# Optimization experiments

Measured on AMD Instinct MI355X. Metric: run time of the kernel, lower is better.

Reference implementation:

```python
import jax, jax.numpy as jnp
import numpy as np

B, S, D, H, DFF = 4, 2048, 512, 8, 2048
DK = D // H
EPS = 1e-6
NEG = -1.0e9


def _linear(x, w, b):
    return x @ w.T + b


def _layernorm(x, gamma, bias):
    # torch.var default is unbiased (ddof=1); gamma/bias are scalars
    mean = jnp.mean(x, axis=-1, keepdims=True)
    var = jnp.var(x, axis=-1, keepdims=True, ddof=1)
    return gamma * (x - mean) / jnp.sqrt(var + EPS) + bias


def setup_inputs() -> dict:
    key = jax.random.key(0)
    ks = jax.random.split(key, 16)
    sc = 0.02
    inp = {
        "x": jax.random.normal(ks[0], (B, S, D), jnp.float32),
        "mask": jax.random.randint(ks[1], (B, 1, 1, S), 0, 2).astype(jnp.bool_),
        "wq": jax.random.normal(ks[2], (D, D), jnp.float32) * sc,
        "bq": jnp.zeros((D,), jnp.float32),
        "wk": jax.random.normal(ks[3], (D, D), jnp.float32) * sc,
        "bk": jnp.zeros((D,), jnp.float32),
        "wv": jax.random.normal(ks[4], (D, D), jnp.float32) * sc,
        "bv": jnp.zeros((D,), jnp.float32),
        "wo": jax.random.normal(ks[5], (D, D), jnp.float32) * sc,
        "bo": jnp.zeros((D,), jnp.float32),
        "w1": jax.random.normal(ks[6], (DFF, D), jnp.float32) * sc,
        "b1": jnp.zeros((DFF,), jnp.float32),
        "w2": jax.random.normal(ks[7], (D, DFF), jnp.float32) * sc,
        "b2": jnp.zeros((D,), jnp.float32),
        "g1": jnp.ones((), jnp.float32),
        "beta1": jnp.zeros((), jnp.float32),
        "g2": jnp.ones((), jnp.float32),
        "beta2": jnp.zeros((), jnp.float32),
    }
    return inp


def reference(x, mask, wq, bq, wk, bk, wv, bv, wo, bo, w1, b1, w2, b2, g1, beta1, g2, beta2):
    # --- multi-head self-attention ---
    q = _linear(x, wq, bq).reshape(B, S, H, DK)
    k = _linear(x, wk, bk).reshape(B, S, H, DK)
    v = _linear(x, wv, bv).reshape(B, S, H, DK)
    scores = jnp.einsum("bqhd,bkhd->bhqk", q, k) / jnp.sqrt(jnp.float32(DK))
    scores = jnp.where(mask, NEG, scores)  # masked_fill_ where mask is True
    attn = jax.nn.softmax(scores, axis=-1)
    o = jnp.einsum("bhqk,bkhd->bqhd", attn, v).reshape(B, S, D)
    attn_out = _linear(o, wo, bo)
    # skip connection 1: x + norm(sublayer_out)  (dropout = identity at inference)
    y = x + _layernorm(attn_out, g1, beta1)
    # --- feed-forward ---
    ff = _linear(jax.nn.relu(_linear(y, w1, b1)), w2, b2)
    # skip connection 2
    return y + _layernorm(ff, g2, beta2)
```

## Files before the change

kernel.cpp:

```cpp
#include <hip/hip_runtime.h>
#include <hip/hip_bf16.h>
#include <math.h>

#define B_ 4
#define S_ 2048
#define D_ 512
#define H_ 8
#define DK_ 64
#define DFF_ 2048
#define NEG_ (-1.0e9f)
#define EPS_ 1e-6f

typedef __attribute__((ext_vector_type(8))) short bf16x8;
typedef __attribute__((ext_vector_type(4))) float f32x4;

__device__ inline unsigned short f2bf(float f) {
    unsigned u = __float_as_uint(f);
    unsigned r = u + 0x7FFFu + ((u >> 16) & 1u);
    return (unsigned short)(r >> 16);
}

__device__ inline f32x4 mfma16(bf16x8 a, bf16x8 b, f32x4 c) {
    return __builtin_amdgcn_mfma_f32_16x16x32_bf16(a, b, c, 0, 0, 0);
}

__device__ inline void gload16(const void* g, void* l) {
    __builtin_amdgcn_global_load_lds(
        (const __attribute__((address_space(1))) unsigned int*)g,
        (__attribute__((address_space(3))) unsigned int*)l, 16, 0, 0);
}
__device__ inline void gload4(const void* g, void* l) {
    __builtin_amdgcn_global_load_lds(
        (const __attribute__((address_space(1))) unsigned int*)g,
        (__attribute__((address_space(3))) unsigned int*)l, 4, 0, 0);
}

__global__ void mask_canon_kernel(const unsigned char* __restrict__ mraw,
                                  float* __restrict__ mb) {
    __shared__ int s_bad;
    int tid = threadIdx.x;
    if (tid == 0) s_bad = 0;
    __syncthreads();
    const unsigned int* w = (const unsigned int*)mraw;
    int bad = 0;
    for (int i = tid; i < (B_ * S_) / 4; i += 256) {
        unsigned int v = w[i];
        if (!(v == 0u || v == 1u || v == 0x3F800000u)) bad = 1;
    }
    if (bad) atomicOr(&s_bad, 1);
    __syncthreads();
    int i = blockIdx.x * 256 + tid;
    if (s_bad) {
        for (; i < B_ * S_; i += 2048) mb[i] = mraw[i] ? NEG_ : 0.f;
    } else {
        for (; i < B_ * S_; i += 2048) mb[i] = w[i] ? NEG_ : 0.f;
    }
}

__global__ __launch_bounds__(256) void convert_all_kernel(
    const float* __restrict__ x,  const float* __restrict__ wq,
    const float* __restrict__ wk, const float* __restrict__ wv,
    const float* __restrict__ wo, const float* __restrict__ w1,
    const float* __restrict__ w2,
    unsigned short* __restrict__ xb, unsigned short* __restrict__ wqkvb,
    unsigned short* __restrict__ wob, unsigned short* __restrict__ w1b,
    unsigned short* __restrict__ w2b)
{
    int i = blockIdx.x * 256 + threadIdx.x;
    const float* src; unsigned short* dst; int off; float s = 1.f;
    if (i < 1048576)      { src = x;  dst = xb;             off = i;           }
    else if (i < 1114112) { src = wq; dst = wqkvb;          off = i - 1048576; s = 0.125f; }
    else if (i < 1179648) { src = wk; dst = wqkvb + 262144; off = i - 1114112; }
    else if (i < 1245184) { src = wv; dst = wqkvb + 524288; off = i - 1179648; }
    else if (i < 1310720) { src = wo; dst = wob;            off = i - 1245184; }
    else if (i < 1572864) { src = w1; dst = w1b;            off = i - 1310720; }
    else                  { src = w2; dst = w2b;            off = i - 1572864; }
    float4 v = reinterpret_cast<const float4*>(src)[off];
    ushort4 o;
    o.x = f2bf(v.x * s); o.y = f2bf(v.y * s); o.z = f2bf(v.z * s); o.w = f2bf(v.w * s);
    reinterpret_cast<ushort4*>(dst)[off] = o;
}

template<int BM, int BN, bool RELU, bool OUT_BF16>
__global__ __launch_bounds__(256) void gemm_mfma(
    const unsigned short* __restrict__ A, const unsigned short* __restrict__ W,
    const float* __restrict__ bias, void* __restrict__ Cout,
    int M, int N, int K)
{
    constexpr int FM = BM / 32;
    constexpr int FN = BN / 32;
    __shared__ unsigned short Asl[BM * 64];
    __shared__ unsigned short Bsl[BN * 64];

    const int tid = threadIdx.x;
    const int w = tid >> 6, lane = tid & 63;
    const int lr = lane & 15, lg = lane >> 4;
    const int wm = w >> 1, wn = w & 1;
    const int m0 = blockIdx.y * BM, n0 = blockIdx.x * BN;
    const int srow = lane >> 3;
    const int schunk = lane & 7;

    f32x4 acc[FM][FN] = {};

    for (int k0 = 0; k0 < K; k0 += 64) {
        __syncthreads();
        #pragma unroll
        for (int j = 0; j < BM / 32; ++j) {
            int instr = w * (BM / 32) + j;
            int row = instr * 8 + srow;
            const unsigned short* src =
                A + (size_t)(m0 + row) * K + k0 + ((schunk ^ (row & 7)) * 8);
            gload16(src, &Asl[instr * 512]);
        }
        #pragma unroll
        for (int j = 0; j < BN / 32; ++j) {
            int instr = w * (BN / 32) + j;
            int row = instr * 8 + srow;
            const unsigned short* src =
                W + (size_t)(n0 + row) * K + k0 + ((schunk ^ (row & 7)) * 8);
            gload16(src, &Bsl[instr * 512]);
        }
        __syncthreads();

        bf16x8 af[FM][2], bfr[FN][2];
        #pragma unroll
        for (int m = 0; m < FM; ++m)
            #pragma unroll
            for (int ko = 0; ko < 2; ++ko) {
                int row = wm * (FM * 16) + m * 16 + lr;
                int slot = (lg + 4 * ko) ^ (row & 7);
                af[m][ko] = *(const bf16x8*)&Asl[row * 64 + slot * 8];
            }
        #pragma unroll
        for (int n = 0; n < FN; ++n)
            #pragma unroll
            for (int ko = 0; ko < 2; ++ko) {
                int row = wn * (FN * 16) + n * 16 + lr;
                int slot = (lg + 4 * ko) ^ (row & 7);
                bfr[n][ko] = *(const bf16x8*)&Bsl[row * 64 + slot * 8];
            }
        #pragma unroll
        for (int m = 0; m < FM; ++m)
            #pragma unroll
            for (int n = 0; n < FN; ++n)
                #pragma unroll
                for (int ko = 0; ko < 2; ++ko)
                    acc[m][n] = mfma16(af[m][ko], bfr[n][ko], acc[m][n]);
    }

    #pragma unroll
    for (int n = 0; n < FN; ++n) {
        int col = n0 + wn * (FN * 16) + n * 16 + lr;
        float bv = bias[col];
        #pragma unroll
        for (int m = 0; m < FM; ++m) {
            int rowb = m0 + wm * (FM * 16) + m * 16 + lg * 4;
            #pragma unroll
            for (int r = 0; r < 4; ++r) {
                float v = acc[m][n][r] + bv;
                if (RELU) v = fmaxf(v, 0.f);
                if (OUT_BF16)
                    ((unsigned short*)Cout)[(size_t)(rowb + r) * N + col] = f2bf(v);
                else
                    ((float*)Cout)[(size_t)(rowb + r) * N + col] = v;
            }
        }
    }
}

__global__ __launch_bounds__(256) void gemm_qkv(
    const unsigned short* __restrict__ A, const unsigned short* __restrict__ W,
    const float* __restrict__ bqp, const float* __restrict__ bkp,
    const float* __restrict__ bvp, unsigned short* __restrict__ QKb,
    unsigned short* __restrict__ VTg)
{
    constexpr int K = 512;
    __shared__ unsigned short Asl[128 * 64];
    __shared__ unsigned short Bsl[128 * 64];

    const int tid = threadIdx.x;
    const int w = tid >> 6, lane = tid & 63;
    const int lr = lane & 15, lg = lane >> 4;
    const int wm = w >> 1, wn = w & 1;
    const int m0 = blockIdx.y * 128, n0 = blockIdx.x * 128;
    const int srow = lane >> 3;
    const int schunk = lane & 7;

    f32x4 acc[4][4] = {};

    for (int k0 = 0; k0 < K; k0 += 64) {
        __syncthreads();
        #pragma unroll
        for (int j = 0; j < 4; ++j) {
            int instr = w * 4 + j;
            int row = instr * 8 + srow;
            gload16(A + (size_t)(m0 + row) * K + k0 + ((schunk ^ (row & 7)) * 8),
                    &Asl[instr * 512]);
            gload16(W + (size_t)(n0 + row) * K + k0 + ((schunk ^ (row & 7)) * 8),
                    &Bsl[instr * 512]);
        }
        __syncthreads();

        bf16x8 af[4][2], bfr[4][2];
        #pragma unroll
        for (int m = 0; m < 4; ++m)
            #pragma unroll
            for (int ko = 0; ko < 2; ++ko) {
                int row = wm * 64 + m * 16 + lr;
                int slot = (lg + 4 * ko) ^ (row & 7);
                af[m][ko] = *(const bf16x8*)&Asl[row * 64 + slot * 8];
            }
        #pragma unroll
        for (int n = 0; n < 4; ++n)
            #pragma unroll
            for (int ko = 0; ko < 2; ++ko) {
                int row = wn * 64 + n * 16 + lr;
                int slot = (lg + 4 * ko) ^ (row & 7);
                bfr[n][ko] = *(const bf16x8*)&Bsl[row * 64 + slot * 8];
            }
        #pragma unroll
        for (int m = 0; m < 4; ++m)
            #pragma unroll
            for (int n = 0; n < 4; ++n)
                #pragma unroll
                for (int ko = 0; ko < 2; ++ko)
                    acc[m][n] = mfma16(af[m][ko], bfr[n][ko], acc[m][n]);
    }

    if (n0 < 1024) {
        #pragma unroll
        for (int n = 0; n < 4; ++n) {
            int col = n0 + wn * 64 + n * 16 + lr;
            float bv = (col < 512) ? bqp[col] * 0.125f : bkp[col - 512];
            #pragma unroll
            for (int m = 0; m < 4; ++m) {
                int rowb = m0 + wm * 64 + m * 16 + lg * 4;
                #pragma unroll
                for (int r = 0; r < 4; ++r)
                    QKb[(size_t)(rowb + r) * 1024 + col] = f2bf(acc[m][n][r] + bv);
            }
        }
    } else {
        #pragma unroll
        for (int n = 0; n < 4; ++n) {
            int col = n0 + wn * 64 + n * 16 + lr;
            int dfull = col - 1024;
            int hh = dfull >> 6, dd = dfull & 63;
            float bv = bvp[dfull];
            #pragma unroll
            for (int m = 0; m < 4; ++m) {
                int rowb = m0 + wm * 64 + m * 16 + lg * 4;
                int bb = rowb >> 11;
                int s = rowb & 2047;
                ushort4 pk;
                pk.x = f2bf(acc[m][n][0] + bv);
                pk.y = f2bf(acc[m][n][1] + bv);
                pk.z = f2bf(acc[m][n][2] + bv);
                pk.w = f2bf(acc[m][n][3] + bv);
                *(ushort4*)&VTg[(((size_t)bb * 8 + hh) * 64 + dd) * 2048 + s] = pk;
            }
        }
    }
}

__global__ __launch_bounds__(256, 4) void attn_mfma3(
    const unsigned short* __restrict__ QKb, const unsigned short* __restrict__ VTg,
    const float* __restrict__ mb, unsigned short* __restrict__ Ob)
{
    __shared__ unsigned short Ks[64 * 64];
    __shared__ unsigned short VTs[64 * 64];
    __shared__ unsigned short Ps[4 * 16 * 64];
    __shared__ float Ms[64];

    const int tid = threadIdx.x;
    const int w = tid >> 6, lane = tid & 63;
    const int lr = lane & 15, lg = lane >> 4;
    const int flat = blockIdx.x + 32 * (blockIdx.y + 8 * blockIdx.z);
    const int nf = (flat & 7) * 128 + (flat >> 3);
    const int q0 = (nf & 31) * 64;
    const int bh = nf >> 5;
    const int h = bh & 7, b = bh >> 3;
    const int srow = lane >> 3;
    const int sc_x = (lane & 7) ^ srow;
    unsigned short* PsW = &Ps[w * 1024];

    bf16x8 qf[2];
    #pragma unroll
    for (int ko = 0; ko < 2; ++ko)
        qf[ko] = *(const bf16x8*)(QKb +
            (size_t)(b * S_ + q0 + w * 16 + lr) * 1024 + h * 64 + ko * 32 + lg * 8);

    f32x4 od[4] = {};
    float m_run = -INFINITY;
    float l_run = 0.f;

    for (int kv0 = 0; kv0 < S_; kv0 += 64) {
        __syncthreads();
        #pragma unroll
        for (int j = 0; j < 2; ++j) {
            int rl = w * 16 + j * 8 + srow;
            gload16(QKb + (size_t)(b * S_ + kv0 + rl) * 1024 + 512 + h * 64 + sc_x * 8,
                    &Ks[(w * 2 + j) * 512]);
            gload16(VTg + ((size_t)bh * 64 + rl) * 2048 + kv0 + sc_x * 8,
                    &VTs[(w * 2 + j) * 512]);
        }
        if (w == 0) gload4(mb + (size_t)b * S_ + kv0 + lane, Ms);
        __syncthreads();

        f32x4 st[4] = {};
        #pragma unroll
        for (int ko = 0; ko < 2; ++ko)
            #pragma unroll
            for (int n = 0; n < 4; ++n) {
                bf16x8 kf = *(const bf16x8*)
                    &Ks[(n * 16 + lr) * 64 + (((lg + 4 * ko) ^ (lr & 7)) * 8)];
                st[n] = mfma16(kf, qf[ko], st[n]);
            }

        float mtp = -INFINITY;
        #pragma unroll
        for (int n = 0; n < 4; ++n) {
            f32x4 mbr = *(const f32x4*)&Ms[n * 16 + lg * 4];
            #pragma unroll
            for (int r = 0; r < 4; ++r) {
                float v = st[n][r] + mbr[r];
                st[n][r] = v;
                mtp = fmaxf(mtp, v);
            }
        }

        if (__any(mtp > m_run + 4.f)) {
            float mt = mtp;
            mt = fmaxf(mt, __shfl_xor(mt, 16));
            mt = fmaxf(mt, __shfl_xor(mt, 32));
            float mnew = fmaxf(m_run, mt);
            float scl = __expf(m_run - mnew);
            m_run = mnew;
            l_run *= scl;
            #pragma unroll
            for (int r = 0; r < 4; ++r) {
                float sr = __shfl(scl, lg * 4 + r);
                #pragma unroll
                for (int nd = 0; nd < 4; ++nd) od[nd][r] *= sr;
            }
        }

        float psum = 0.f;
        #pragma unroll
        for (int n = 0; n < 4; ++n) {
            float p0 = __expf(st[n][0] - m_run);
            float p1 = __expf(st[n][1] - m_run);
            float p2 = __expf(st[n][2] - m_run);
            float p3 = __expf(st[n][3] - m_run);
            psum += (p0 + p1) + (p2 + p3);
            ushort4 pk;
            pk.x = f2bf(p0); pk.y = f2bf(p1); pk.z = f2bf(p2); pk.w = f2bf(p3);
            int chunk = (2 * n + (lg >> 1)) ^ (lr & 7);
            *(ushort4*)&PsW[lr * 64 + chunk * 8 + (lg & 1) * 4] = pk;
        }
        psum += __shfl_xor(psum, 16);
        psum += __shfl_xor(psum, 32);
        l_run += psum;

        #pragma unroll
        for (int ko = 0; ko < 2; ++ko) {
            int slotx = ((lg + 4 * ko) ^ (lr & 7)) * 8;
            bf16x8 pa = *(const bf16x8*)&PsW[lr * 64 + slotx];
            #pragma unroll
            for (int nd = 0; nd < 4; ++nd) {
                bf16x8 vf = *(const bf16x8*)&VTs[(nd * 16 + lr) * 64 + slotx];
                od[nd] = mfma16(pa, vf, od[nd]);
            }
        }
    }

    float linv = 1.f / l_run;
    #pragma unroll
    for (int r = 0; r < 4; ++r) {
        float iv = __shfl(linv, lg * 4 + r);
        size_t row = (size_t)(b * S_ + q0 + w * 16 + lg * 4 + r);
        #pragma unroll
        for (int nd = 0; nd < 4; ++nd)
            Ob[row * 512 + h * 64 + nd * 16 + lr] = f2bf(od[nd][r] * iv);
    }
}

__global__ __launch_bounds__(256) void add_ln_kernel(
    const float* __restrict__ x, const float* __restrict__ a,
    const float* __restrict__ g, const float* __restrict__ beta,
    float* __restrict__ y, unsigned short* __restrict__ ybf)
{
    int rowid = blockIdx.x;
    int tid = threadIdx.x;
    const float2 a2 = reinterpret_cast<const float2*>(a + (size_t)rowid * D_)[tid];
    float s = a2.x + a2.y;
    float ss = a2.x * a2.x + a2.y * a2.y;
    #pragma unroll
    for (int off = 32; off > 0; off >>= 1) {
        s += __shfl_down(s, off);
        ss += __shfl_down(ss, off);
    }
    __shared__ float ws_s[4], ws_ss[4];
    __shared__ float s_mean, s_rstd;
    int wave = tid >> 6, lane = tid & 63;
    if (lane == 0) { ws_s[wave] = s; ws_ss[wave] = ss; }
    __syncthreads();
    if (tid == 0) {
        float st = ws_s[0] + ws_s[1] + ws_s[2] + ws_s[3];
        float sst = ws_ss[0] + ws_ss[1] + ws_ss[2] + ws_ss[3];
        float mean = st / (float)D_;
        float var = (sst - (float)D_ * mean * mean) / (float)(D_ - 1);
        s_mean = mean;
        s_rstd = rsqrtf(var + EPS_);
    }
    __syncthreads();
    float mean = s_mean, rstd = s_rstd, gg = g[0], bb = beta[0];
    const float2 x2 = reinterpret_cast<const float2*>(x + (size_t)rowid * D_)[tid];
    float2 o;
    o.x = x2.x + gg * (a2.x - mean) * rstd + bb;
    o.y = x2.y + gg * (a2.y - mean) * rstd + bb;
    reinterpret_cast<float2*>(y + (size_t)rowid * D_)[tid] = o;
    if (ybf) {
        ushort2 ob; ob.x = f2bf(o.x); ob.y = f2bf(o.y);
        reinterpret_cast<ushort2*>(ybf + (size_t)rowid * D_)[tid] = ob;
    }
}

extern "C" void kernel_launch(void* const* d_in, const int* in_sizes, int n_in,
                              void* d_out, int out_size, void* d_ws, size_t ws_size,
                              hipStream_t stream) {
    const float* x  = (const float*)d_in[0];
    const unsigned char* mask = (const unsigned char*)d_in[1];
    const float* wq = (const float*)d_in[2];
    const float* bq = (const float*)d_in[3];
    const float* wk = (const float*)d_in[4];
    const float* bk = (const float*)d_in[5];
    const float* wv = (const float*)d_in[6];
    const float* bv = (const float*)d_in[7];
    const float* wo = (const float*)d_in[8];
    const float* bo = (const float*)d_in[9];
    const float* w1 = (const float*)d_in[10];
    const float* b1 = (const float*)d_in[11];
    const float* w2 = (const float*)d_in[12];
    const float* b2 = (const float*)d_in[13];
    const float* g1 = (const float*)d_in[14];
    const float* be1 = (const float*)d_in[15];
    const float* g2 = (const float*)d_in[16];
    const float* be2 = (const float*)d_in[17];
    float* out = (float*)d_out;
    char* base = (char*)d_ws;

    const size_t MS = (size_t)B_ * S_;
    unsigned short* QKb  = (unsigned short*)(base);
    unsigned short* VTg  = (unsigned short*)(base + 16777216);
    unsigned short* Ob   = (unsigned short*)(base + 25165824);
    unsigned short* ff1  = (unsigned short*)(base);
    float*          att  = (float*)(base + 33554432);
    float*          ff2  = att;
    float*          y    = (float*)(base + 50331648);
    unsigned short* ybf  = (unsigned short*)(base + 67108864);
    unsigned short* xb   = (unsigned short*)(base + 75497472);
    unsigned short* wqkvb= (unsigned short*)(base + 83886080);
    unsigned short* wob  = (unsigned short*)(base + 85458944);
    unsigned short* w1b  = (unsigned short*)(base + 85983232);
    unsigned short* w2b  = (unsigned short*)(base + 88080384);
    float*          mbv  = (float*)(base + 90183680);

    dim3 blk(256);
    mask_canon_kernel<<<8, blk, 0, stream>>>(mask, mbv);

    convert_all_kernel<<<7168, blk, 0, stream>>>(
        x, wq, wk, wv, wo, w1, w2, xb, wqkvb, wob, w1b, w2b);

    gemm_qkv<<<dim3(12, MS / 128), blk, 0, stream>>>(
        xb, wqkvb, bq, bk, bv, QKb, VTg);

    attn_mfma3<<<dim3(S_ / 64, H_, B_), blk, 0, stream>>>(QKb, VTg, mbv, Ob);

    gemm_mfma<128,64,false,false><<<dim3(D_/64, MS/128), blk, 0, stream>>>(
        Ob, wob, bo, att, MS, D_, D_);

    add_ln_kernel<<<dim3((unsigned)MS), blk, 0, stream>>>(x, att, g1, be1, y, ybf);

    gemm_mfma<128,128,true,true><<<dim3(DFF_/128, MS/128), blk, 0, stream>>>(
        ybf, w1b, b1, ff1, MS, DFF_, D_);
    gemm_mfma<128,64,false,false><<<dim3(D_/64, MS/128), blk, 0, stream>>>(
        ff1, w2b, b2, ff2, MS, D_, DFF_);

    add_ln_kernel<<<dim3((unsigned)MS), blk, 0, stream>>>(y, ff2, g2, be2, out, nullptr);
}
```

Before: 296.8 us.

## Double-buffer attention K/V tiles, use exp2 softmax, and remap GEMM blocks across XCDs

The attention kernel now double-buffers K and V^T tiles in LDS and prefetches the next tile while computing the current one, so one barrier per iteration replaces two. The mask bias is read straight from global memory instead of staged through LDS. The softmax runs in base 2: log2(e) is folded into the Q weight and bias scaling, exp2f replaces __expf, and the rescale threshold is raised. Probabilities are packed to bf16 with paired conversions, and the GEMM block indices are permuted so neighbouring tiles spread across the 8 XCDs for better L2 locality. The cost is doubled LDS for K/V, which may limit occupancy.

```diff
diff --git a/kernel.cpp b/kernel.cpp
--- a/kernel.cpp
+++ b/kernel.cpp
@@ -10,6 +10,7 @@
 #define DFF_ 2048
 #define NEG_ (-1.0e9f)
 #define EPS_ 1e-6f
+#define LOG2E_ 1.4426950408889634f
 
 typedef __attribute__((ext_vector_type(8))) short bf16x8;
 typedef __attribute__((ext_vector_type(4))) float f32x4;
@@ -20,6 +21,13 @@
     return (unsigned short)(r >> 16);
 }
 
+__device__ inline unsigned int packbf2(float a, float b) {
+    __hip_bfloat162 h = __float22bfloat162_rn(float2{a, b});
+    unsigned int u;
+    __builtin_memcpy(&u, &h, 4);
+    return u;
+}
+
 __device__ inline f32x4 mfma16(bf16x8 a, bf16x8 b, f32x4 c) {
     return __builtin_amdgcn_mfma_f32_16x16x32_bf16(a, b, c, 0, 0, 0);
 }
@@ -28,11 +36,6 @@
     __builtin_amdgcn_global_load_lds(
         (const __attribute__((address_space(1))) unsigned int*)g,
         (__attribute__((address_space(3))) unsigned int*)l, 16, 0, 0);
-}
-__device__ inline void gload4(const void* g, void* l) {
-    __builtin_amdgcn_global_load_lds(
-        (const __attribute__((address_space(1))) unsigned int*)g,
-        (__attribute__((address_space(3))) unsigned int*)l, 4, 0, 0);
 }
 
 __global__ void mask_canon_kernel(const unsigned char* __restrict__ mraw,
@@ -69,7 +72,7 @@
     int i = blockIdx.x * 256 + threadIdx.x;
     const float* src; unsigned short* dst; int off; float s = 1.f;
     if (i < 1048576)      { src = x;  dst = xb;             off = i;           }
-    else if (i < 1114112) { src = wq; dst = wqkvb;          off = i - 1048576; s = 0.125f; }
+    else if (i < 1114112) { src = wq; dst = wqkvb;          off = i - 1048576; s = 0.125f * LOG2E_; }
     else if (i < 1179648) { src = wk; dst = wqkvb + 262144; off = i - 1114112; }
     else if (i < 1245184) { src = wv; dst = wqkvb + 524288; off = i - 1179648; }
     else if (i < 1310720) { src = wo; dst = wob;            off = i - 1245184; }
@@ -96,7 +99,11 @@
     const int w = tid >> 6, lane = tid & 63;
     const int lr = lane & 15, lg = lane >> 4;
     const int wm = w >> 1, wn = w & 1;
-    const int m0 = blockIdx.y * BM, n0 = blockIdx.x * BN;
+    const int gx = gridDim.x;
+    const int flat = blockIdx.y * gx + blockIdx.x;
+    const int cpx = (gx * gridDim.y) >> 3;
+    const int nf = (flat & 7) * cpx + (flat >> 3);
+    const int m0 = (nf / gx) * BM, n0 = (nf % gx) * BN;
     const int srow = lane >> 3;
     const int schunk = lane & 7;
 
@@ -182,7 +189,9 @@
     const int w = tid >> 6, lane = tid & 63;
     const int lr = lane & 15, lg = lane >> 4;
     const int wm = w >> 1, wn = w & 1;
-    const int m0 = blockIdx.y * 128, n0 = blockIdx.x * 128;
+    const int flat = blockIdx.y * 12 + blockIdx.x;
+    const int nf = (flat & 7) * 96 + (flat >> 3);
+    const int m0 = (nf / 12) * 128, n0 = (nf % 12) * 128;
     const int srow = lane >> 3;
     const int schunk = lane & 7;
 
@@ -231,7 +240,7 @@
         #pragma unroll
         for (int n = 0; n < 4; ++n) {
             int col = n0 + wn * 64 + n * 16 + lr;
-            float bv = (col < 512) ? bqp[col] * 0.125f : bkp[col - 512];
+            float bv = (col < 512) ? bqp[col] * (0.125f * LOG2E_) : bkp[col - 512];
             #pragma unroll
             for (int m = 0; m < 4; ++m) {
                 int rowb = m0 + wm * 64 + m * 16 + lg * 4;
@@ -263,14 +272,28 @@
     }
 }
 
-__global__ __launch_bounds__(256, 4) void attn_mfma3(
+__device__ inline void stage_kv(const unsigned short* __restrict__ QKb,
+                                const unsigned short* __restrict__ VTg,
+                                unsigned short* ksDst, unsigned short* vtDst,
+                                int b, int bh, int h, int kv0,
+                                int w, int srow, int sc_x) {
+    #pragma unroll
+    for (int j = 0; j < 2; ++j) {
+        int rl = w * 16 + j * 8 + srow;
+        gload16(QKb + (size_t)(b * S_ + kv0 + rl) * 1024 + 512 + h * 64 + sc_x * 8,
+                ksDst + (w * 2 + j) * 512);
+        gload16(VTg + ((size_t)bh * 64 + rl) * 2048 + kv0 + sc_x * 8,
+                vtDst + (w * 2 + j) * 512);
+    }
+}
+
+__global__ __launch_bounds__(256, 4) void attn_mfma4(
     const unsigned short* __restrict__ QKb, const unsigned short* __restrict__ VTg,
     const float* __restrict__ mb, unsigned short* __restrict__ Ob)
 {
-    __shared__ unsigned short Ks[64 * 64];
-    __shared__ unsigned short VTs[64 * 64];
+    __shared__ unsigned short Ks[2][64 * 64];
+    __shared__ unsigned short VTs[2][64 * 64];
     __shared__ unsigned short Ps[4 * 16 * 64];
-    __shared__ float Ms[64];
 
     const int tid = threadIdx.x;
     const int w = tid >> 6, lane = tid & 63;
@@ -294,18 +317,19 @@
     float m_run = -INFINITY;
     float l_run = 0.f;
 
+    stage_kv(QKb, VTg, Ks[0], VTs[0], b, bh, h, 0, w, srow, sc_x);
+    __syncthreads();
+
+    int cur = 0;
     for (int kv0 = 0; kv0 < S_; kv0 += 64) {
-        __syncthreads();
-        #pragma unroll
-        for (int j = 0; j < 2; ++j) {
-            int rl = w * 16 + j * 8 + srow;
-            gload16(QKb + (size_t)(b * S_ + kv0 + rl) * 1024 + 512 + h * 64 + sc_x * 8,
-                    &Ks[(w * 2 + j) * 512]);
-            gload16(VTg + ((size_t)bh * 64 + rl) * 2048 + kv0 + sc_x * 8,
-                    &VTs[(w * 2 + j) * 512]);
-        }
-        if (w == 0) gload4(mb + (size_t)b * S_ + kv0 + lane, Ms);
-        __syncthreads();
+        if (kv0 + 64 < S_)
+            stage_kv(QKb, VTg, Ks[cur ^ 1], VTs[cur ^ 1], b, bh, h, kv0 + 64,
+                     w, srow, sc_x);
+
+        f32x4 mbr[4];
+        #pragma unroll
+        for (int n = 0; n < 4; ++n)
+            mbr[n] = *(const f32x4*)&mb[(size_t)b * S_ + kv0 + n * 16 + lg * 4];
 
         f32x4 st[4] = {};
         #pragma unroll
@@ -313,28 +337,26 @@
             #pragma unroll
             for (int n = 0; n < 4; ++n) {
                 bf16x8 kf = *(const bf16x8*)
-                    &Ks[(n * 16 + lr) * 64 + (((lg + 4 * ko) ^ (lr & 7)) * 8)];
+                    &Ks[cur][(n * 16 + lr) * 64 + (((lg + 4 * ko) ^ (lr & 7)) * 8)];
                 st[n] = mfma16(kf, qf[ko], st[n]);
             }
 
         float mtp = -INFINITY;
         #pragma unroll
-        for (int n = 0; n < 4; ++n) {
-            f32x4 mbr = *(const f32x4*)&Ms[n * 16 + lg * 4];
+        for (int n = 0; n < 4; ++n)
             #pragma unroll
             for (int r = 0; r < 4; ++r) {
-                float v = st[n][r] + mbr[r];
+                float v = st[n][r] + mbr[n][r];
                 st[n][r] = v;
                 mtp = fmaxf(mtp, v);
             }
-        }
-
-        if (__any(mtp > m_run + 4.f)) {
+
+        if (__any(mtp > m_run + 8.f)) {
             float mt = mtp;
             mt = fmaxf(mt, __shfl_xor(mt, 16));
             mt = fmaxf(mt, __shfl_xor(mt, 32));
             float mnew = fmaxf(m_run, mt);
-            float scl = __expf(m_run - mnew);
+            float scl = exp2f(m_run - mnew);
             m_run = mnew;
             l_run *= scl;
             #pragma unroll
@@ -348,15 +370,16 @@
         float psum = 0.f;
         #pragma unroll
         for (int n = 0; n < 4; ++n) {
-            float p0 = __expf(st[n][0] - m_run);
-            float p1 = __expf(st[n][1] - m_run);
-            float p2 = __expf(st[n][2] - m_run);
-            float p3 = __expf(st[n][3] - m_run);
+            float p0 = exp2f(st[n][0] - m_run);
+            float p1 = exp2f(st[n][1] - m_run);
+            float p2 = exp2f(st[n][2] - m_run);
+            float p3 = exp2f(st[n][3] - m_run);
             psum += (p0 + p1) + (p2 + p3);
-            ushort4 pk;
-            pk.x = f2bf(p0); pk.y = f2bf(p1); pk.z = f2bf(p2); pk.w = f2bf(p3);
+            uint2 pk;
+            pk.x = packbf2(p0, p1);
+            pk.y = packbf2(p2, p3);
             int chunk = (2 * n + (lg >> 1)) ^ (lr & 7);
-            *(ushort4*)&PsW[lr * 64 + chunk * 8 + (lg & 1) * 4] = pk;
+            *(uint2*)&PsW[lr * 64 + chunk * 8 + (lg & 1) * 4] = pk;
         }
         psum += __shfl_xor(psum, 16);
         psum += __shfl_xor(psum, 32);
@@ -368,10 +391,12 @@
             bf16x8 pa = *(const bf16x8*)&PsW[lr * 64 + slotx];
             #pragma unroll
             for (int nd = 0; nd < 4; ++nd) {
-                bf16x8 vf = *(const bf16x8*)&VTs[(nd * 16 + lr) * 64 + slotx];
+                bf16x8 vf = *(const bf16x8*)&VTs[cur][(nd * 16 + lr) * 64 + slotx];
                 od[nd] = mfma16(pa, vf, od[nd]);
             }
         }
+        __syncthreads();
+        cur ^= 1;
     }
 
     float linv = 1.f / l_run;
@@ -475,7 +500,7 @@
     gemm_qkv<<<dim3(12, MS / 128), blk, 0, stream>>>(
         xb, wqkvb, bq, bk, bv, QKb, VTg);
 
-    attn_mfma3<<<dim3(S_ / 64, H_, B_), blk, 0, stream>>>(QKb, VTg, mbv, Ob);
+    attn_mfma4<<<dim3(S_ / 64, H_, B_), blk, 0, stream>>>(QKb, VTg, mbv, Ob);
 
     gemm_mfma<128,64,false,false><<<dim3(D_/64, MS/128), blk, 0, stream>>>(
         Ob, wob, bo, att, MS, D_, D_);
```

New measurement: 300.3 us. About the same (+1.2%).

## Merge prep kernels, fold log2e into Q, swizzle GEMM blocks, wave-per-row layernorm

Applied to the files above, without the earlier changes.

Merges mask canonicalization and bf16 conversion into one launch, saving a kernel launch. Folds log2(e) into the Q weight and bias scale so attention can use exp2f, and seeds the score accumulator with the mask bias instead of adding it afterwards. It also raises the rescale threshold, remaps GEMM block indices across XCDs for cache locality, and rewrites add+layernorm to one wave per row using float4 loads and no shared-memory reduction. The lazy rescale threshold of 8 in log2 units allows larger unnormalized partial sums, which adds some precision risk.

```diff
diff --git a/kernel.cpp b/kernel.cpp
--- a/kernel.cpp
+++ b/kernel.cpp
@@ -10,6 +10,7 @@
 #define DFF_ 2048
 #define NEG_ (-1.0e9f)
 #define EPS_ 1e-6f
+#define LOG2E_ 1.4426950408889634f
 
 typedef __attribute__((ext_vector_type(8))) short bf16x8;
 typedef __attribute__((ext_vector_type(4))) float f32x4;
@@ -35,29 +36,8 @@
         (__attribute__((address_space(3))) unsigned int*)l, 4, 0, 0);
 }
 
-__global__ void mask_canon_kernel(const unsigned char* __restrict__ mraw,
-                                  float* __restrict__ mb) {
-    __shared__ int s_bad;
-    int tid = threadIdx.x;
-    if (tid == 0) s_bad = 0;
-    __syncthreads();
-    const unsigned int* w = (const unsigned int*)mraw;
-    int bad = 0;
-    for (int i = tid; i < (B_ * S_) / 4; i += 256) {
-        unsigned int v = w[i];
-        if (!(v == 0u || v == 1u || v == 0x3F800000u)) bad = 1;
-    }
-    if (bad) atomicOr(&s_bad, 1);
-    __syncthreads();
-    int i = blockIdx.x * 256 + tid;
-    if (s_bad) {
-        for (; i < B_ * S_; i += 2048) mb[i] = mraw[i] ? NEG_ : 0.f;
-    } else {
-        for (; i < B_ * S_; i += 2048) mb[i] = w[i] ? NEG_ : 0.f;
-    }
-}
-
-__global__ __launch_bounds__(256) void convert_all_kernel(
+__global__ __launch_bounds__(256) void prep_kernel(
+    const unsigned char* __restrict__ mraw, float* __restrict__ mb,
     const float* __restrict__ x,  const float* __restrict__ wq,
     const float* __restrict__ wk, const float* __restrict__ wv,
     const float* __restrict__ wo, const float* __restrict__ w1,
@@ -66,10 +46,31 @@
     unsigned short* __restrict__ wob, unsigned short* __restrict__ w1b,
     unsigned short* __restrict__ w2b)
 {
-    int i = blockIdx.x * 256 + threadIdx.x;
+    int tid = threadIdx.x;
+    if (blockIdx.x < 8) {
+        __shared__ int s_bad;
+        if (tid == 0) s_bad = 0;
+        __syncthreads();
+        const unsigned int* w = (const unsigned int*)mraw;
+        int bad = 0;
+        for (int i = tid; i < (B_ * S_) / 4; i += 256) {
+            unsigned int v = w[i];
+            if (!(v == 0u || v == 1u || v == 0x3F800000u)) bad = 1;
+        }
+        if (bad) atomicOr(&s_bad, 1);
+        __syncthreads();
+        int i = blockIdx.x * 256 + tid;
+        if (s_bad) {
+            for (; i < B_ * S_; i += 2048) mb[i] = mraw[i] ? NEG_ : 0.f;
+        } else {
+            for (; i < B_ * S_; i += 2048) mb[i] = w[i] ? NEG_ : 0.f;
+        }
+        return;
+    }
+    int i = (blockIdx.x - 8) * 256 + tid;
     const float* src; unsigned short* dst; int off; float s = 1.f;
     if (i < 1048576)      { src = x;  dst = xb;             off = i;           }
-    else if (i < 1114112) { src = wq; dst = wqkvb;          off = i - 1048576; s = 0.125f; }
+    else if (i < 1114112) { src = wq; dst = wqkvb;          off = i - 1048576; s = 0.125f * LOG2E_; }
     else if (i < 1179648) { src = wk; dst = wqkvb + 262144; off = i - 1114112; }
     else if (i < 1245184) { src = wv; dst = wqkvb + 524288; off = i - 1179648; }
     else if (i < 1310720) { src = wo; dst = wob;            off = i - 1245184; }
@@ -96,7 +97,11 @@
     const int w = tid >> 6, lane = tid & 63;
     const int lr = lane & 15, lg = lane >> 4;
     const int wm = w >> 1, wn = w & 1;
-    const int m0 = blockIdx.y * BM, n0 = blockIdx.x * BN;
+    const int gx = gridDim.x;
+    const int flat = blockIdx.y * gx + blockIdx.x;
+    const int cpx = (gx * gridDim.y) >> 3;
+    const int nf = (flat & 7) * cpx + (flat >> 3);
+    const int m0 = (nf / gx) * BM, n0 = (nf % gx) * BN;
     const int srow = lane >> 3;
     const int schunk = lane & 7;
 
@@ -182,7 +187,9 @@
     const int w = tid >> 6, lane = tid & 63;
     const int lr = lane & 15, lg = lane >> 4;
     const int wm = w >> 1, wn = w & 1;
-    const int m0 = blockIdx.y * 128, n0 = blockIdx.x * 128;
+    const int flat = blockIdx.y * 12 + blockIdx.x;
+    const int nf = (flat & 7) * 96 + (flat >> 3);
+    const int m0 = (nf / 12) * 128, n0 = (nf % 12) * 128;
     const int srow = lane >> 3;
     const int schunk = lane & 7;
 
@@ -231,7 +238,7 @@
         #pragma unroll
         for (int n = 0; n < 4; ++n) {
             int col = n0 + wn * 64 + n * 16 + lr;
-            float bv = (col < 512) ? bqp[col] * 0.125f : bkp[col - 512];
+            float bv = (col < 512) ? bqp[col] * (0.125f * LOG2E_) : bkp[col - 512];
             #pragma unroll
             for (int m = 0; m < 4; ++m) {
                 int rowb = m0 + wm * 64 + m * 16 + lg * 4;
@@ -263,7 +270,7 @@
     }
 }
 
-__global__ __launch_bounds__(256, 4) void attn_mfma3(
+__global__ __launch_bounds__(256, 4) void attn_mfma5(
     const unsigned short* __restrict__ QKb, const unsigned short* __restrict__ VTg,
     const float* __restrict__ mb, unsigned short* __restrict__ Ob)
 {
@@ -307,7 +314,10 @@
         if (w == 0) gload4(mb + (size_t)b * S_ + kv0 + lane, Ms);
         __syncthreads();
 
-        f32x4 st[4] = {};
+        f32x4 st[4];
+        #pragma unroll
+        for (int n = 0; n < 4; ++n)
+            st[n] = *(const f32x4*)&Ms[n * 16 + lg * 4];
         #pragma unroll
         for (int ko = 0; ko < 2; ++ko)
             #pragma unroll
@@ -319,22 +329,17 @@
 
         float mtp = -INFINITY;
         #pragma unroll
-        for (int n = 0; n < 4; ++n) {
-            f32x4 mbr = *(const f32x4*)&Ms[n * 16 + lg * 4];
-            #pragma unroll
-            for (int r = 0; r < 4; ++r) {
-                float v = st[n][r] + mbr[r];
-                st[n][r] = v;
-                mtp = fmaxf(mtp, v);
-            }
-        }
-
-        if (__any(mtp > m_run + 4.f)) {
+        for (int n = 0; n < 4; ++n)
+            #pragma unroll
+            for (int r = 0; r < 4; ++r)
+                mtp = fmaxf(mtp, st[n][r]);
+
+        if (__any(mtp > m_run + 8.f)) {
             float mt = mtp;
             mt = fmaxf(mt, __shfl_xor(mt, 16));
             mt = fmaxf(mt, __shfl_xor(mt, 32));
             float mnew = fmaxf(m_run, mt);
-            float scl = __expf(m_run - mnew);
+            float scl = exp2f(m_run - mnew);
             m_run = mnew;
             l_run *= scl;
             #pragma unroll
@@ -348,10 +353,10 @@
         float psum = 0.f;
         #pragma unroll
         for (int n = 0; n < 4; ++n) {
-            float p0 = __expf(st[n][0] - m_run);
-            float p1 = __expf(st[n][1] - m_run);
-            float p2 = __expf(st[n][2] - m_run);
-            float p3 = __expf(st[n][3] - m_run);
+            float p0 = exp2f(st[n][0] - m_run);
+            float p1 = exp2f(st[n][1] - m_run);
+            float p2 = exp2f(st[n][2] - m_run);
+            float p3 = exp2f(st[n][3] - m_run);
             psum += (p0 + p1) + (p2 + p3);
             ushort4 pk;
             pk.x = f2bf(p0); pk.y = f2bf(p1); pk.z = f2bf(p2); pk.w = f2bf(p3);
@@ -385,44 +390,46 @@
     }
 }
 
-__global__ __launch_bounds__(256) void add_ln_kernel(
+__global__ __launch_bounds__(256) void add_ln2_kernel(
     const float* __restrict__ x, const float* __restrict__ a,
     const float* __restrict__ g, const float* __restrict__ beta,
     float* __restrict__ y, unsigned short* __restrict__ ybf)
 {
-    int rowid = blockIdx.x;
-    int tid = threadIdx.x;
-    const float2 a2 = reinterpret_cast<const float2*>(a + (size_t)rowid * D_)[tid];
-    float s = a2.x + a2.y;
-    float ss = a2.x * a2.x + a2.y * a2.y;
+    const int wv = threadIdx.x >> 6, lane = threadIdx.x & 63;
+    const size_t row = (size_t)blockIdx.x * 4 + wv;
+    const float4* a4 = (const float4*)(a + row * D_);
+    float4 va0 = a4[lane * 2], va1 = a4[lane * 2 + 1];
+    float s  = (va0.x + va0.y) + (va0.z + va0.w) + (va1.x + va1.y) + (va1.z + va1.w);
+    float ss = (va0.x * va0.x + va0.y * va0.y) + (va0.z * va0.z + va0.w * va0.w)
+             + (va1.x * va1.x + va1.y * va1.y) + (va1.z * va1.z + va1.w * va1.w);
     #pragma unroll
     for (int off = 32; off > 0; off >>= 1) {
-        s += __shfl_down(s, off);
-        ss += __shfl_down(ss, off);
-    }
-    __shared__ float ws_s[4], ws_ss[4];
-    __shared__ float s_mean, s_rstd;
-    int wave = tid >> 6, lane = tid & 63;
-    if (lane == 0) { ws_s[wave] = s; ws_ss[wave] = ss; }
-    __syncthreads();
-    if (tid == 0) {
-        float st = ws_s[0] + ws_s[1] + ws_s[2] + ws_s[3];
-        float sst = ws_ss[0] + ws_ss[1] + ws_ss[2] + ws_ss[3];
-        float mean = st / (float)D_;
-        float var = (sst - (float)D_ * mean * mean) / (float)(D_ - 1);
-        s_mean = mean;
-        s_rstd = rsqrtf(var + EPS_);
-    }
-    __syncthreads();
-    float mean = s_mean, rstd = s_rstd, gg = g[0], bb = beta[0];
-    const float2 x2 = reinterpret_cast<const float2*>(x + (size_t)rowid * D_)[tid];
-    float2 o;
-    o.x = x2.x + gg * (a2.x - mean) * rstd + bb;
-    o.y = x2.y + gg * (a2.y - mean) * rstd + bb;
-    reinterpret_cast<float2*>(y + (size_t)rowid * D_)[tid] = o;
+        s  += __shfl_xor(s, off);
+        ss += __shfl_xor(ss, off);
+    }
+    float mean = s * (1.f / (float)D_);
+    float var  = (ss - (float)D_ * mean * mean) * (1.f / (float)(D_ - 1));
+    float rstd = rsqrtf(var + EPS_);
+    float gg = g[0], bb = beta[0];
+    const float4* x4 = (const float4*)(x + row * D_);
+    float4 vx0 = x4[lane * 2], vx1 = x4[lane * 2 + 1];
+    float4 o0, o1;
+    o0.x = vx0.x + gg * (va0.x - mean) * rstd + bb;
+    o0.y = vx0.y + gg * (va0.y - mean) * rstd + bb;
+    o0.z = vx0.z + gg * (va0.z - mean) * rstd + bb;
+    o0.w = vx0.w + gg * (va0.w - mean) * rstd + bb;
+    o1.x = vx1.x + gg * (va1.x - mean) * rstd + bb;
+    o1.y = vx1.y + gg * (va1.y - mean) * rstd + bb;
+    o1.z = vx1.z + gg * (va1.z - mean) * rstd + bb;
+    o1.w = vx1.w + gg * (va1.w - mean) * rstd + bb;
+    ((float4*)(y + row * D_))[lane * 2]     = o0;
+    ((float4*)(y + row * D_))[lane * 2 + 1] = o1;
     if (ybf) {
-        ushort2 ob; ob.x = f2bf(o.x); ob.y = f2bf(o.y);
-        reinterpret_cast<ushort2*>(ybf + (size_t)rowid * D_)[tid] = ob;
+        ushort4 u0, u1;
+        u0.x = f2bf(o0.x); u0.y = f2bf(o0.y); u0.z = f2bf(o0.z); u0.w = f2bf(o0.w);
+        u1.x = f2bf(o1.x); u1.y = f2bf(o1.y); u1.z = f2bf(o1.z); u1.w = f2bf(o1.w);
+        ((ushort4*)(ybf + row * D_))[lane * 2]     = u0;
+        ((ushort4*)(ybf + row * D_))[lane * 2 + 1] = u1;
     }
 }
 
@@ -467,25 +474,23 @@
     float*          mbv  = (float*)(base + 90183680);
 
     dim3 blk(256);
-    mask_canon_kernel<<<8, blk, 0, stream>>>(mask, mbv);
-
-    convert_all_kernel<<<7168, blk, 0, stream>>>(
-        x, wq, wk, wv, wo, w1, w2, xb, wqkvb, wob, w1b, w2b);
+    prep_kernel<<<7176, blk, 0, stream>>>(
+        mask, mbv, x, wq, wk, wv, wo, w1, w2, xb, wqkvb, wob, w1b, w2b);
 
     gemm_qkv<<<dim3(12, MS / 128), blk, 0, stream>>>(
         xb, wqkvb, bq, bk, bv, QKb, VTg);
 
-    attn_mfma3<<<dim3(S_ / 64, H_, B_), blk, 0, stream>>>(QKb, VTg, mbv, Ob);
+    attn_mfma5<<<dim3(S_ / 64, H_, B_), blk, 0, stream>>>(QKb, VTg, mbv, Ob);
 
     gemm_mfma<128,64,false,false><<<dim3(D_/64, MS/128), blk, 0, stream>>>(
         Ob, wob, bo, att, MS, D_, D_);
 
-    add_ln_kernel<<<dim3((unsigned)MS), blk, 0, stream>>>(x, att, g1, be1, y, ybf);
+    add_ln2_kernel<<<dim3((unsigned)(MS / 4)), blk, 0, stream>>>(x, att, g1, be1, y, ybf);
 
     gemm_mfma<128,128,true,true><<<dim3(DFF_/128, MS/128), blk, 0, stream>>>(
         ybf, w1b, b1, ff1, MS, DFF_, D_);
     gemm_mfma<128,64,false,false><<<dim3(D_/64, MS/128), blk, 0, stream>>>(
         ff1, w2b, b2, ff2, MS, D_, DFF_);
 
-    add_ln_kernel<<<dim3((unsigned)MS), blk, 0, stream>>>(y, ff2, g2, be2, out, nullptr);
-}
+    add_ln2_kernel<<<dim3((unsigned)(MS / 4)), blk, 0, stream>>>(y, ff2, g2, be2, out, nullptr);
+}
```

Measured after the change: 296.1 us. No clear change (-0.2%).
